# Kernel optimization log

Measured on AMD Instinct MI355X. Metric: run time of the kernel, lower is better.

The kernel has to match this reference:

```python
import jax, jax.numpy as jnp
import numpy as np

N_HEAD = 12
NEG_INF = -1e30


def setup_inputs() -> dict:
    key = jax.random.key(0)
    ks = jax.random.split(key, 12)
    bs, q_len, c_len, d = 2, 2048, 2048, 768
    s = 1.0 / np.sqrt(d)
    return {
        "query": jax.random.normal(ks[0], (bs, q_len, d), jnp.float32),
        "context": jax.random.normal(ks[1], (bs, c_len, d), jnp.float32),
        "c_mask": jax.random.randint(ks[2], (bs, c_len), 0, 2, jnp.int32),
        "Wq_w": jax.random.normal(ks[3], (d, d), jnp.float32) * s,
        "Wq_b": jnp.zeros((d,), jnp.float32),
        "Wk_w": jax.random.normal(ks[4], (d, d), jnp.float32) * s,
        "Wk_b": jnp.zeros((d,), jnp.float32),
        "Wv_w": jax.random.normal(ks[5], (d, d), jnp.float32) * s,
        "Wv_b": jnp.zeros((d,), jnp.float32),
        "fc_w": jax.random.normal(ks[6], (d, d), jnp.float32) * s,
        "fc_b": jnp.zeros((d,), jnp.float32),
    }


def reference(query, context, c_mask, Wq_w, Wq_b, Wk_w, Wk_b, Wv_w, Wv_b, fc_w, fc_b):
    bs, q_len, d = query.shape
    c_len = context.shape[1]
    d_k = d // N_HEAD
    a = 1.0 / np.sqrt(d_k)

    # QKV projections (torch Linear: y = x @ W.T + b), split into heads
    q = (query @ Wq_w.T + Wq_b).reshape(bs, q_len, N_HEAD, d_k)
    k = (context @ Wk_w.T + Wk_b).reshape(bs, c_len, N_HEAD, d_k)
    v = (context @ Wv_w.T + Wv_b).reshape(bs, c_len, N_HEAD, d_k)

    # scores [bs, n_head, q_len, c_len]
    s = jnp.einsum('bqhd,bchd->bhqc', q, k) * a

    # mask_logits: s * m + (1 - m) * -1e30, mask broadcast over heads and q
    m = c_mask.astype(s.dtype)[:, None, None, :]
    s = s * m + (1.0 - m) * NEG_INF

    p = jax.nn.softmax(s, axis=-1)  # dropout p=0.0 -> identity

    out = jnp.einsum('bhqc,bchd->bqhd', p, v).reshape(bs, q_len, d)
    return out @ fc_w.T + fc_b
```

## Files before the change

### kernel.cpp

```cpp
#include <hip/hip_runtime.h>
#include <cstdint>

#define D_MODEL 768
#define NH      12
#define DKH     64
#define SEQ     2048
#define BS      2
#define MROWS   (BS*SEQ)

typedef __bf16 bf16x8 __attribute__((ext_vector_type(8)));
typedef float  f32x4  __attribute__((ext_vector_type(4)));
typedef unsigned int u32_as1 __attribute__((address_space(1)));
typedef unsigned int u32_as3 __attribute__((address_space(3)));

__device__ __forceinline__ void gld16(const void* g, void* l) {
  __builtin_amdgcn_global_load_lds((const u32_as1*)g, (u32_as3*)l, 16, 0, 0);
}
__device__ __forceinline__ unsigned short f2bf(float x) {
  return __builtin_bit_cast(unsigned short, (__bf16)x);
}

__global__ void cvt2(const float* __restrict__ a, const float* __restrict__ b,
                     unsigned short* __restrict__ oa, unsigned short* __restrict__ ob) {
  const float* in = blockIdx.y ? b : a;
  unsigned short* out = blockIdx.y ? ob : oa;
  int i = blockIdx.x * 256 + threadIdx.x;
  float4 v = reinterpret_cast<const float4*>(in)[i];
  ushort4 o; o.x = f2bf(v.x); o.y = f2bf(v.y); o.z = f2bf(v.z); o.w = f2bf(v.w);
  reinterpret_cast<ushort4*>(out)[i] = o;
}
__global__ void cvt4(const float* __restrict__ a, const float* __restrict__ b,
                     const float* __restrict__ c, const float* __restrict__ d,
                     unsigned short* __restrict__ oa, unsigned short* __restrict__ ob,
                     unsigned short* __restrict__ oc, unsigned short* __restrict__ od) {
  const float* in; unsigned short* out;
  switch (blockIdx.y) {
    case 0: in = a; out = oa; break;
    case 1: in = b; out = ob; break;
    case 2: in = c; out = oc; break;
    default: in = d; out = od; break;
  }
  int i = blockIdx.x * 256 + threadIdx.x;
  float4 v = reinterpret_cast<const float4*>(in)[i];
  ushort4 o; o.x = f2bf(v.x); o.y = f2bf(v.y); o.z = f2bf(v.z); o.w = f2bf(v.w);
  reinterpret_cast<ushort4*>(out)[i] = o;
}

template<bool OUT_F32>
__device__ __forceinline__ void gemm64x128_body(
    const unsigned short* __restrict__ A, const unsigned short* __restrict__ B,
    const float* __restrict__ bias, int biasRow, void* __restrict__ Cout,
    int ldc, int m0, int n0)
{
  __shared__ alignas(16) char sA[2][8192];
  __shared__ alignas(16) char sB[2][16384];
  const int tid = threadIdx.x;
  const int w = tid >> 6, l = tid & 63;
  const int g16 = l >> 4, c16 = l & 15;
  const int wr = (w >> 1) * 32, wc = (w & 1) * 64;

  auto stageA = [&](int kt, char* dst) {
#pragma unroll
    for (int i = 0; i < 2; i++) {
      int ch = w * 2 + i;
      int X = ch * 1024 + l * 16;
      int row = X >> 7;
      int sl = ((X >> 4) & 7) ^ (row & 7);
      gld16(A + (size_t)(m0 + row) * 768 + kt + sl * 8, dst + ch * 1024);
    }
  };
  auto stageB = [&](int kt, char* dst) {
#pragma unroll
    for (int i = 0; i < 4; i++) {
      int ch = w * 4 + i;
      int X = ch * 1024 + l * 16;
      int row = X >> 7;
      int sl = ((X >> 4) & 7) ^ (row & 7);
      gld16(B + (size_t)(n0 + row) * 768 + kt + sl * 8, dst + ch * 1024);
    }
  };

  f32x4 acc[2][4];
#pragma unroll
  for (int m = 0; m < 2; m++)
#pragma unroll
    for (int n = 0; n < 4; n++) acc[m][n] = f32x4{0.f, 0.f, 0.f, 0.f};

  stageA(0, sA[0]);
  stageB(0, sB[0]);
  __syncthreads();
  int cur = 0;
  for (int kt = 0; kt < 768; kt += 64) {
    if (kt + 64 < 768) {
      stageA(kt + 64, sA[cur ^ 1]);
      stageB(kt + 64, sB[cur ^ 1]);
    }
    __builtin_amdgcn_s_setprio(1);
#pragma unroll
    for (int kk = 0; kk < 2; kk++) {
      bf16x8 af[2], bq[4];
#pragma unroll
      for (int m = 0; m < 2; m++) {
        int row = wr + m * 16 + c16, slot = kk * 4 + g16;
        af[m] = *(const bf16x8*)(sA[cur] + row * 128 + ((slot ^ (row & 7)) << 4));
      }
#pragma unroll
      for (int n = 0; n < 4; n++) {
        int row = wc + n * 16 + c16, slot = kk * 4 + g16;
        bq[n] = *(const bf16x8*)(sB[cur] + row * 128 + ((slot ^ (row & 7)) << 4));
      }
#pragma unroll
      for (int m = 0; m < 2; m++)
#pragma unroll
        for (int n = 0; n < 4; n++)
          acc[m][n] = __builtin_amdgcn_mfma_f32_16x16x32_bf16(af[m], bq[n], acc[m][n], 0, 0, 0);
    }
    __builtin_amdgcn_s_setprio(0);
    __syncthreads();
    cur ^= 1;
  }

#pragma unroll
  for (int m = 0; m < 2; m++)
#pragma unroll
    for (int n = 0; n < 4; n++)
#pragma unroll
      for (int r = 0; r < 4; r++) {
        int row = m0 + wr + m * 16 + g16 * 4 + r;
        int col = n0 + wc + n * 16 + c16;
        float v = acc[m][n][r] + (biasRow ? bias[row] : bias[col]);
        if constexpr (OUT_F32) ((float*)Cout)[(size_t)row * ldc + col] = v;
        else ((unsigned short*)Cout)[(size_t)row * ldc + col] = f2bf(v);
      }
}

__global__ __launch_bounds__(256, 2) void gemm_qkv(
    const unsigned short* __restrict__ q_bf, const unsigned short* __restrict__ c_bf,
    const unsigned short* __restrict__ wq, const unsigned short* __restrict__ wk,
    const unsigned short* __restrict__ wv,
    const float* __restrict__ bq, const float* __restrict__ bk,
    const float* __restrict__ bv,
    unsigned short* __restrict__ Qb, unsigned short* __restrict__ Kb,
    unsigned short* __restrict__ Vtb)
{
  const int x = blockIdx.x;
  const int lin = (x & 7) * 48 + (x >> 3);
  if (blockIdx.y == 0) {
    gemm64x128_body<false>(q_bf, wq, bq, 0, Qb, 768, (lin / 6) * 64, (lin % 6) * 128);
  } else if (blockIdx.y == 1) {
    gemm64x128_body<false>(c_bf, wk, bk, 0, Kb, 768, (lin / 6) * 64, (lin % 6) * 128);
  } else {
    gemm64x128_body<false>(wv, c_bf, bv, 1, Vtb, 4096, (lin % 12) * 64, (lin / 12) * 128);
  }
}

__global__ __launch_bounds__(256, 2) void gemm_fc(
    const unsigned short* __restrict__ Ob, const unsigned short* __restrict__ wf,
    const float* __restrict__ fb, float* __restrict__ out)
{
  const int x = blockIdx.x;
  const int lin = (x & 7) * 48 + (x >> 3);
  gemm64x128_body<true>(Ob, wf, fb, 0, out, 768, (lin / 6) * 64, (lin % 6) * 128);
}

__global__ __launch_bounds__(256, 4) void attn_kernel(
    const unsigned short* __restrict__ Qb, const unsigned short* __restrict__ Kb,
    const unsigned short* __restrict__ Vt, const int* __restrict__ cmask,
    unsigned short* __restrict__ Ob)
{
  __shared__ alignas(16) char sK[2][8192];
  __shared__ alignas(16) char sV[2][8192];
  __shared__ alignas(16) char sP[8192];
  const int tid = threadIdx.x, w = tid >> 6, l = tid & 63;
  const int g16 = l >> 4, c16 = l & 15;
  const int flat = blockIdx.x;
  const int xcd = flat & 7, sidx = flat >> 3;
  const int p = xcd + 8 * (sidx >> 5);
  const int qt = sidx & 31;
  const int h = p % 12, b = p / 12;
  const int qrow0 = b * SEQ + qt * 64;
  const int crow0 = b * SEQ;

  bf16x8 qa[2];
  {
    const unsigned short* qp =
        Qb + (size_t)(qrow0 + w * 16 + c16) * D_MODEL + h * DKH + g16 * 8;
    qa[0] = *(const bf16x8*)(qp);
    qa[1] = *(const bf16x8*)(qp + 32);
  }

  auto stageK = [&](int ct, int buf) {
#pragma unroll
    for (int i = 0; i < 2; i++) {
      int ch = w * 2 + i;
      int X = ch * 1024 + l * 16;
      int row = X >> 7;
      int sl = ((X >> 4) & 7) ^ (row & 7);
      gld16(Kb + (size_t)(crow0 + ct + row) * D_MODEL + h * DKH + sl * 8,
            sK[buf] + ch * 1024);
    }
  };
  auto stageV = [&](int ct, int buf) {
#pragma unroll
    for (int i = 0; i < 2; i++) {
      int ch = w * 2 + i;
      int X = ch * 1024 + l * 16;
      int row = X >> 7;
      int sl = ((X >> 4) & 7) ^ (row & 7);
      gld16(Vt + (size_t)(h * DKH + row) * (size_t)MROWS + crow0 + ct + sl * 8,
            sV[buf] + ch * 1024);
    }
  };

  f32x4 accO[4], accL;
#pragma unroll
  for (int n = 0; n < 4; n++) accO[n] = f32x4{0.f, 0.f, 0.f, 0.f};
  accL = f32x4{0.f, 0.f, 0.f, 0.f};
  const __bf16 one = (__bf16)1.0f;
  const bf16x8 vones = {one, one, one, one, one, one, one, one};

  stageK(0, 0); stageV(0, 0);
  __syncthreads();
  int cur = 0;

  for (int ct = 0; ct < SEQ; ct += 64) {
    if (ct + 64 < SEQ) { stageK(ct + 64, cur ^ 1); stageV(ct + 64, cur ^ 1); }

    int mk[4];
#pragma unroll
    for (int n = 0; n < 4; n++) mk[n] = cmask[crow0 + ct + n * 16 + c16];

    f32x4 s[4];
#pragma unroll
    for (int n = 0; n < 4; n++) s[n] = f32x4{0.f, 0.f, 0.f, 0.f};
    __builtin_amdgcn_s_setprio(1);
#pragma unroll
    for (int kk = 0; kk < 2; kk++) {
      bf16x8 kf[4];
#pragma unroll
      for (int n = 0; n < 4; n++) {
        int row = n * 16 + c16, slot = kk * 4 + g16;
        kf[n] = *(const bf16x8*)(sK[cur] + row * 128 + ((slot ^ (row & 7)) << 4));
      }
#pragma unroll
      for (int n = 0; n < 4; n++)
        s[n] = __builtin_amdgcn_mfma_f32_16x16x32_bf16(qa[kk], kf[n], s[n], 0, 0, 0);
    }
    __builtin_amdgcn_s_setprio(0);

#pragma unroll
    for (int r = 0; r < 4; r++) {
      int prow = g16 * 4 + r;
#pragma unroll
      for (int n = 0; n < 4; n++) {
        float pv = mk[n] ? __expf(s[n][r] * 0.125f) : 0.f;
        int slot = n * 2 + (c16 >> 3);
        int addr = w * 2048 + prow * 128 + ((slot ^ (prow & 7)) << 4) + (c16 & 7) * 2;
        *(__bf16*)(sP + addr) = (__bf16)pv;
      }
    }

    __builtin_amdgcn_s_setprio(1);
#pragma unroll
    for (int kk = 0; kk < 2; kk++) {
      bf16x8 pa, vf[4];
      {
        int prow = c16, slot = kk * 4 + g16;
        pa = *(const bf16x8*)(sP + w * 2048 + prow * 128 + ((slot ^ (prow & 7)) << 4));
      }
#pragma unroll
      for (int n = 0; n < 4; n++) {
        int vrow = n * 16 + c16, slot = kk * 4 + g16;
        vf[n] = *(const bf16x8*)(sV[cur] + vrow * 128 + ((slot ^ (vrow & 7)) << 4));
      }
#pragma unroll
      for (int n = 0; n < 4; n++)
        accO[n] = __builtin_amdgcn_mfma_f32_16x16x32_bf16(pa, vf[n], accO[n], 0, 0, 0);
      accL = __builtin_amdgcn_mfma_f32_16x16x32_bf16(pa, vones, accL, 0, 0, 0);
    }
    __builtin_amdgcn_s_setprio(0);

    __syncthreads();
    cur ^= 1;
  }

#pragma unroll
  for (int r = 0; r < 4; r++) {
    float inv = 1.0f / accL[r];
#pragma unroll
    for (int n = 0; n < 4; n++) {
      int row = qrow0 + w * 16 + g16 * 4 + r;
      int col = h * DKH + n * 16 + c16;
      Ob[(size_t)row * D_MODEL + col] = f2bf(accO[n][r] * inv);
    }
  }
}

extern "C" void kernel_launch(void* const* d_in, const int* in_sizes, int n_in,
                              void* d_out, int out_size, void* d_ws, size_t ws_size,
                              hipStream_t stream) {
  const float* query   = (const float*)d_in[0];
  const float* context = (const float*)d_in[1];
  const int*   cmask   = (const int*)d_in[2];
  const float* Wq_w = (const float*)d_in[3];
  const float* Wq_b = (const float*)d_in[4];
  const float* Wk_w = (const float*)d_in[5];
  const float* Wk_b = (const float*)d_in[6];
  const float* Wv_w = (const float*)d_in[7];
  const float* Wv_b = (const float*)d_in[8];
  const float* fc_w = (const float*)d_in[9];
  const float* fc_b = (const float*)d_in[10];
  float* out = (float*)d_out;

  unsigned short* ws   = (unsigned short*)d_ws;
  const size_t NQ = (size_t)MROWS * D_MODEL;
  const size_t NW = (size_t)D_MODEL * D_MODEL;
  unsigned short* q_bf = ws;
  unsigned short* c_bf = q_bf + NQ;
  unsigned short* Qb   = c_bf + NQ;
  unsigned short* Kb   = Qb + NQ;
  unsigned short* Vtb  = Kb + NQ;
  unsigned short* Ob   = Vtb + NQ;
  unsigned short* wq   = Ob + NQ;
  unsigned short* wk   = wq + NW;
  unsigned short* wv   = wk + NW;
  unsigned short* wf   = wv + NW;

  cvt2<<<dim3(NQ / 4 / 256, 2), 256, 0, stream>>>(query, context, q_bf, c_bf);
  cvt4<<<dim3(NW / 4 / 256, 4), 256, 0, stream>>>(Wq_w, Wk_w, Wv_w, fc_w, wq, wk, wv, wf);

  gemm_qkv<<<dim3(384, 3), 256, 0, stream>>>(
      q_bf, c_bf, wq, wk, wv, Wq_b, Wk_b, Wv_b, Qb, Kb, Vtb);

  attn_kernel<<<768, 256, 0, stream>>>(Qb, Kb, Vtb, cmask, Ob);

  gemm_fc<<<384, 256, 0, stream>>>(Ob, wf, fc_b, out);
}
```

Measured before the change: 97.47 us.

## Fold softmax scale and key mask into projections, use exp2 in attention

Scales Q by log2(e)/sqrt(dk) in the QKV GEMM epilogue so the attention loop can call raw exp2 without a multiply. Zeroes masked columns of V^T in the projection epilogue and computes the softmax denominator with an MFMA against a bf16 mask vector, removing the per-element mask select from the inner loop. Adds a small kernel that converts the mask to bf16, writing into the now-dead q_bf buffer. The risk is that exp of masked scores is still computed and could overflow, and it relies on row maxima staying small since there is no max subtraction.

```diff
diff --git a/kernel.cpp b/kernel.cpp
--- a/kernel.cpp
+++ b/kernel.cpp
@@ -46,11 +46,16 @@
   reinterpret_cast<ushort4*>(out)[i] = o;
 }
 
+__global__ void mask_bf(const int* __restrict__ m, unsigned short* __restrict__ o) {
+  int i = blockIdx.x * 256 + threadIdx.x;
+  o[i] = f2bf(m[i] ? 1.0f : 0.0f);
+}
+
 template<bool OUT_F32>
 __device__ __forceinline__ void gemm64x128_body(
     const unsigned short* __restrict__ A, const unsigned short* __restrict__ B,
     const float* __restrict__ bias, int biasRow, void* __restrict__ Cout,
-    int ldc, int m0, int n0)
+    int ldc, int m0, int n0, float outScale, const int* __restrict__ colMask)
 {
   __shared__ alignas(16) char sA[2][8192];
   __shared__ alignas(16) char sB[2][16384];
@@ -128,29 +133,35 @@
       for (int r = 0; r < 4; r++) {
         int row = m0 + wr + m * 16 + g16 * 4 + r;
         int col = n0 + wc + n * 16 + c16;
-        float v = acc[m][n][r] + (biasRow ? bias[row] : bias[col]);
+        float v = (acc[m][n][r] + (biasRow ? bias[row] : bias[col])) * outScale;
+        if (colMask) v *= (float)colMask[col];
         if constexpr (OUT_F32) ((float*)Cout)[(size_t)row * ldc + col] = v;
         else ((unsigned short*)Cout)[(size_t)row * ldc + col] = f2bf(v);
       }
 }
+
+#define QSCALE 0.1803368801111f
 
 __global__ __launch_bounds__(256, 2) void gemm_qkv(
     const unsigned short* __restrict__ q_bf, const unsigned short* __restrict__ c_bf,
     const unsigned short* __restrict__ wq, const unsigned short* __restrict__ wk,
     const unsigned short* __restrict__ wv,
     const float* __restrict__ bq, const float* __restrict__ bk,
-    const float* __restrict__ bv,
+    const float* __restrict__ bv, const int* __restrict__ cmask,
     unsigned short* __restrict__ Qb, unsigned short* __restrict__ Kb,
     unsigned short* __restrict__ Vtb)
 {
   const int x = blockIdx.x;
   const int lin = (x & 7) * 48 + (x >> 3);
   if (blockIdx.y == 0) {
-    gemm64x128_body<false>(q_bf, wq, bq, 0, Qb, 768, (lin / 6) * 64, (lin % 6) * 128);
+    gemm64x128_body<false>(q_bf, wq, bq, 0, Qb, 768, (lin / 6) * 64, (lin % 6) * 128,
+                           QSCALE, nullptr);
   } else if (blockIdx.y == 1) {
-    gemm64x128_body<false>(c_bf, wk, bk, 0, Kb, 768, (lin / 6) * 64, (lin % 6) * 128);
+    gemm64x128_body<false>(c_bf, wk, bk, 0, Kb, 768, (lin / 6) * 64, (lin % 6) * 128,
+                           1.0f, nullptr);
   } else {
-    gemm64x128_body<false>(wv, c_bf, bv, 1, Vtb, 4096, (lin % 12) * 64, (lin / 12) * 128);
+    gemm64x128_body<false>(wv, c_bf, bv, 1, Vtb, 4096, (lin % 12) * 64, (lin / 12) * 128,
+                           1.0f, cmask);
   }
 }
 
@@ -160,12 +171,13 @@
 {
   const int x = blockIdx.x;
   const int lin = (x & 7) * 48 + (x >> 3);
-  gemm64x128_body<true>(Ob, wf, fb, 0, out, 768, (lin / 6) * 64, (lin % 6) * 128);
+  gemm64x128_body<true>(Ob, wf, fb, 0, out, 768, (lin / 6) * 64, (lin % 6) * 128,
+                        1.0f, nullptr);
 }
 
 __global__ __launch_bounds__(256, 4) void attn_kernel(
     const unsigned short* __restrict__ Qb, const unsigned short* __restrict__ Kb,
-    const unsigned short* __restrict__ Vt, const int* __restrict__ cmask,
+    const unsigned short* __restrict__ Vt, const unsigned short* __restrict__ maskbf,
     unsigned short* __restrict__ Ob)
 {
   __shared__ alignas(16) char sK[2][8192];
@@ -216,8 +228,6 @@
 #pragma unroll
   for (int n = 0; n < 4; n++) accO[n] = f32x4{0.f, 0.f, 0.f, 0.f};
   accL = f32x4{0.f, 0.f, 0.f, 0.f};
-  const __bf16 one = (__bf16)1.0f;
-  const bf16x8 vones = {one, one, one, one, one, one, one, one};
 
   stageK(0, 0); stageV(0, 0);
   __syncthreads();
@@ -226,9 +236,10 @@
   for (int ct = 0; ct < SEQ; ct += 64) {
     if (ct + 64 < SEQ) { stageK(ct + 64, cur ^ 1); stageV(ct + 64, cur ^ 1); }
 
-    int mk[4];
-#pragma unroll
-    for (int n = 0; n < 4; n++) mk[n] = cmask[crow0 + ct + n * 16 + c16];
+    bf16x8 mfrag[2];
+#pragma unroll
+    for (int kk = 0; kk < 2; kk++)
+      mfrag[kk] = *(const bf16x8*)(maskbf + crow0 + ct + kk * 32 + g16 * 8);
 
     f32x4 s[4];
 #pragma unroll
@@ -253,7 +264,7 @@
       int prow = g16 * 4 + r;
 #pragma unroll
       for (int n = 0; n < 4; n++) {
-        float pv = mk[n] ? __expf(s[n][r] * 0.125f) : 0.f;
+        float pv = __builtin_amdgcn_exp2f(s[n][r]);
         int slot = n * 2 + (c16 >> 3);
         int addr = w * 2048 + prow * 128 + ((slot ^ (prow & 7)) << 4) + (c16 & 7) * 2;
         *(__bf16*)(sP + addr) = (__bf16)pv;
@@ -276,7 +287,7 @@
 #pragma unroll
       for (int n = 0; n < 4; n++)
         accO[n] = __builtin_amdgcn_mfma_f32_16x16x32_bf16(pa, vf[n], accO[n], 0, 0, 0);
-      accL = __builtin_amdgcn_mfma_f32_16x16x32_bf16(pa, vones, accL, 0, 0, 0);
+      accL = __builtin_amdgcn_mfma_f32_16x16x32_bf16(pa, mfrag[kk], accL, 0, 0, 0);
     }
     __builtin_amdgcn_s_setprio(0);
 
@@ -325,14 +336,17 @@
   unsigned short* wk   = wq + NW;
   unsigned short* wv   = wk + NW;
   unsigned short* wf   = wv + NW;
+  unsigned short* maskbf = q_bf;
 
   cvt2<<<dim3(NQ / 4 / 256, 2), 256, 0, stream>>>(query, context, q_bf, c_bf);
   cvt4<<<dim3(NW / 4 / 256, 4), 256, 0, stream>>>(Wq_w, Wk_w, Wv_w, fc_w, wq, wk, wv, wf);
 
   gemm_qkv<<<dim3(384, 3), 256, 0, stream>>>(
-      q_bf, c_bf, wq, wk, wv, Wq_b, Wk_b, Wv_b, Qb, Kb, Vtb);
-
-  attn_kernel<<<768, 256, 0, stream>>>(Qb, Kb, Vtb, cmask, Ob);
+      q_bf, c_bf, wq, wk, wv, Wq_b, Wk_b, Wv_b, cmask, Qb, Kb, Vtb);
+
+  mask_bf<<<MROWS / 256, 256, 0, stream>>>(cmask, maskbf);
+
+  attn_kernel<<<768, 256, 0, stream>>>(Qb, Kb, Vtb, maskbf, Ob);
 
   gemm_fc<<<384, 256, 0, stream>>>(Ob, wf, fc_b, out);
 }
```

Result: slower. 100.3 us (+2.9%).
